# Optimization experiments

Measured on AMD Instinct MI355X. Metric: run time of the kernel, lower is better.

Reference implementation:

```python
import jax, jax.numpy as jnp
import numpy as np

# --- model dims (ModelArgs defaults) ---
DIM = 1024      # model dim
NH = 12         # n_heads
NOPE = 128      # qk_nope_head_dim
ROPE = 64       # qk_rope_head_dim (32 complex pairs)
QKH = NOPE + ROPE  # 192
VH = 128        # v_head_dim
KVR = 512       # kv_lora_rank
B, S = 4, 2048
EPS = 1e-6
SM_SCALE = QKH ** -0.5  # max_seq_len <= original_seq_len -> no mscale


def setup_inputs() -> dict:
    key = jax.random.key(0)
    ks = jax.random.split(key, 6)
    std = lambda fan_in: 0.02 / np.sqrt(fan_in)
    x = jax.random.normal(ks[0], (B, S, DIM), jnp.float32)
    wq = jax.random.normal(ks[1], (NH * QKH, DIM), jnp.float32) * std(DIM)
    wkv_a = jax.random.normal(ks[2], (KVR + ROPE, DIM), jnp.float32) * std(DIM)
    kv_norm_w = jnp.ones((KVR,), jnp.float32)
    wkv_b = jax.random.normal(ks[3], (NH * (NOPE + VH), KVR), jnp.float32) * std(KVR)
    wo = jax.random.normal(ks[4], (DIM, NH * VH), jnp.float32) * std(NH * VH)
    # rotary freqs_cis for positions [0, S): cos/sin of pos * theta^(-2i/ROPE)
    inv_freq = 1.0 / (10000.0 ** (np.arange(0, ROPE, 2, dtype=np.float32) / ROPE))
    ang = np.outer(np.arange(S, dtype=np.float32), inv_freq)  # [S, 32]
    freqs_cis = jnp.stack([jnp.cos(ang), jnp.sin(ang)], axis=-1).astype(jnp.float32)  # [S,32,2]
    # causal mask [S, S]: -inf above diagonal
    i = jnp.arange(S)
    mask = jnp.where(i[None, :] > i[:, None], -jnp.inf, 0.0).astype(jnp.float32)
    return {"x": x, "wq": wq, "wkv_a": wkv_a, "kv_norm_w": kv_norm_w,
            "wkv_b": wkv_b, "wo": wo, "freqs_cis": freqs_cis, "mask": mask,
            "start_pos": 0}


def rmsnorm(x, w, eps=EPS):
    xf = x.astype(jnp.float32)
    return (xf * jax.lax.rsqrt(jnp.mean(xf * xf, axis=-1, keepdims=True) + eps) * w).astype(x.dtype)


def apply_rope(x, freqs_cis):
    # x: [B, S, H, D]; pairs are consecutive last-dim elements (view_as_complex semantics)
    x2 = x.reshape(*x.shape[:-1], -1, 2)
    xr, xi = x2[..., 0], x2[..., 1]
    fr = freqs_cis[..., 0][None, :, None, :]  # [1, S, 1, D/2]
    fi = freqs_cis[..., 1][None, :, None, :]
    yr = xr * fr - xi * fi
    yi = xr * fi + xi * fr
    return jnp.stack([yr, yi], axis=-1).reshape(x.shape).astype(x.dtype)


def reference(x, wq, wkv_a, kv_norm_w, wkv_b, wo, freqs_cis, mask, start_pos):
    bsz, seqlen, _ = x.shape
    # q projection (q_lora_rank == 0 path)
    q = (x @ wq.T).reshape(bsz, seqlen, NH, QKH)
    q_nope, q_pe = q[..., :NOPE], q[..., NOPE:]
    q_pe = apply_rope(q_pe, freqs_cis)
    # low-rank kv projection
    kv_full = x @ wkv_a.T                       # [B,S,KVR+ROPE]
    kv, k_pe = kv_full[..., :KVR], kv_full[..., KVR:]
    k_pe = apply_rope(k_pe[:, :, None, :], freqs_cis)[:, :, 0, :]  # [B,S,ROPE]
    # absorb k-side of wkv_b into q (MLA absorption)
    wkv_b3 = wkv_b.reshape(NH, NOPE + VH, KVR)
    q_nope = jnp.einsum('bshd,hdc->bshc', q_nope, wkv_b3[:, :NOPE])  # [B,S,H,KVR]
    # latent caches (detached in original module)
    kv_c = jax.lax.stop_gradient(rmsnorm(kv, kv_norm_w))  # [B,S,KVR]
    pe_c = jax.lax.stop_gradient(k_pe)                    # [B,S,ROPE]
    scores = (jnp.einsum('bshc,btc->bsht', q_nope, kv_c)
              + jnp.einsum('bshr,btr->bsht', q_pe, pe_c)) * SM_SCALE
    scores = scores + mask[None, :, None, :]
    attn = jax.nn.softmax(scores.astype(jnp.float32), axis=-1).astype(x.dtype)
    o = jnp.einsum('bsht,btc->bshc', attn, kv_c)           # [B,S,H,KVR]
    o = jnp.einsum('bshc,hdc->bshd', o, wkv_b3[:, NOPE:])  # [B,S,H,VH]
    return o.reshape(bsz, seqlen, NH * VH) @ wo.T           # [B,S,DIM]
```

## Files before the change

### kernel.cpp

```cpp
#include <hip/hip_runtime.h>

typedef __bf16 bf16;
typedef __bf16 bf16x8 __attribute__((ext_vector_type(8)));
typedef __bf16 bf16x4 __attribute__((ext_vector_type(4)));
typedef float floatx4 __attribute__((ext_vector_type(4)));

#define T_TOK 8192
#define SEQ 2048
#define KLD 584
#define SM_SCALE 0.07216878364870323f

__device__ __forceinline__ void dma16(const void* g, void* l) {
  __builtin_amdgcn_global_load_lds(
      (const __attribute__((address_space(1))) unsigned int*)g,
      (__attribute__((address_space(3))) unsigned int*)l, 16, 0, 0);
}

__global__ __launch_bounds__(256) void cast_f32_bf16(const float* __restrict__ in,
                                                     bf16* __restrict__ out, long n4) {
  long i = (long)blockIdx.x * 256 + threadIdx.x;
  if (i >= n4) return;
  float4 v = ((const float4*)in)[i];
  bf16x4 o;
  o[0] = (bf16)v.x; o[1] = (bf16)v.y; o[2] = (bf16)v.z; o[3] = (bf16)v.w;
  ((bf16x4*)out)[i] = o;
}

__global__ __launch_bounds__(256) void cast_wkva_pad(const float* __restrict__ in,
                                                     bf16* __restrict__ out) {
  long i = (long)blockIdx.x * 256 + threadIdx.x;
  int r = (int)(i >> 8);
  bf16x4 o;
  if (r < 576) {
    float4 v = ((const float4*)in)[i];
    o[0] = (bf16)v.x; o[1] = (bf16)v.y; o[2] = (bf16)v.z; o[3] = (bf16)v.w;
  } else {
    o[0] = (bf16)0.f; o[1] = (bf16)0.f; o[2] = (bf16)0.f; o[3] = (bf16)0.f;
  }
  ((bf16x4*)out)[i] = o;
}

__global__ __launch_bounds__(256) void split_wkvb(const float* __restrict__ in,
                                                  bf16* __restrict__ wbnT,
                                                  bf16* __restrict__ wbv) {
  int i = blockIdx.x * 256 + threadIdx.x;
  int h = i >> 17, rem = i & 131071, d = rem >> 9, c = rem & 511;
  bf16 v = (bf16)in[i];
  if (d < 128) wbnT[((h * 512 + c) << 7) + d] = v;
  else         wbv[((h * 128 + (d - 128)) << 9) + c] = v;
}

template <int MODE>
__global__ __launch_bounds__(256) void gemm_bt(
    const bf16* __restrict__ A, const bf16* __restrict__ B, void* __restrict__ Cv,
    int N, int K, int lda, int ldb, int ldc,
    long sA, long sB, long sC,
    const float* __restrict__ freqs, bf16* __restrict__ qn, bf16* __restrict__ qabs) {
  __shared__ alignas(16) bf16 As[128 * 32];
  __shared__ alignas(16) bf16 Bs[128 * 32];
  const int z = blockIdx.z;
  A += (long)z * sA;  B += (long)z * sB;
  const int row0 = blockIdx.y * 128, col0 = blockIdx.x * 128;
  const int tid = threadIdx.x;
  const int w = tid >> 6, l = tid & 63, lm = l & 15, quad = l >> 4;
  const int wr = w >> 1, wc = w & 1;
  floatx4 acc[4][4] = {};

  for (int k0 = 0; k0 < K; k0 += 32) {
    __syncthreads();
#pragma unroll
    for (int i = 0; i < 2; i++) {
      int cid = i * 256 + tid;
      int r = cid >> 2, c8 = (cid & 3) * 8;
      *(bf16x8*)(As + r * 32 + c8) = *(const bf16x8*)(A + (long)(row0 + r) * lda + k0 + c8);
      *(bf16x8*)(Bs + r * 32 + c8) = *(const bf16x8*)(B + (long)(col0 + r) * ldb + k0 + c8);
    }
    __syncthreads();
    bf16x8 af[4], bfr[4];
#pragma unroll
    for (int i = 0; i < 4; i++) {
      af[i]  = *(const bf16x8*)(As + (wr * 64 + i * 16 + lm) * 32 + quad * 8);
      bfr[i] = *(const bf16x8*)(Bs + (wc * 64 + i * 16 + lm) * 32 + quad * 8);
    }
#pragma unroll
    for (int i = 0; i < 4; i++)
#pragma unroll
      for (int j = 0; j < 4; j++)
        acc[i][j] = __builtin_amdgcn_mfma_f32_16x16x32_bf16(af[i], bfr[j], acc[i][j], 0, 0, 0);
  }

#pragma unroll
  for (int i = 0; i < 4; i++) {
#pragma unroll
    for (int j = 0; j < 4; j++) {
#pragma unroll
      for (int r = 0; r < 4; r++) {
        float val = acc[i][j][r];
        float partner = __shfl_xor(val, 1, 64);
        int rr = row0 + wr * 64 + i * 16 + quad * 4 + r;
        int cc = col0 + wc * 64 + j * 16 + lm;
        if (cc < N) {
          if (MODE == 0) {
            ((float*)Cv + (long)z * sC)[(long)rr * ldc + cc] = val;
          } else if (MODE == 1) {
            ((bf16*)Cv + (long)z * sC)[(long)rr * ldc + cc] = (bf16)val;
          } else if (MODE == 3) {
            ((bf16*)Cv + (long)z * sC)[(long)cc * ldc + rr] = (bf16)val;
          } else {
            int s = rr & (SEQ - 1);
            int h = cc / 192, wi = cc % 192;
            if (wi < 128) {
              qn[((long)h * T_TOK + rr) * 128 + wi] = (bf16)(val * SM_SCALE);
            } else {
              int pp = (wi - 128) >> 1;
              float cs = freqs[s * 64 + pp * 2], sn = freqs[s * 64 + pp * 2 + 1];
              float res = ((wi & 1) == 0) ? (val * cs - partner * sn)
                                          : (partner * sn + val * cs);
              qabs[((long)h * T_TOK + rr) * 576 + 512 + (wi - 128)] = (bf16)(res * SM_SCALE);
            }
          }
        }
      }
    }
  }
}

__global__ __launch_bounds__(64) void kvnorm_rope(const float* __restrict__ kvf,
                                                  const float* __restrict__ wnorm,
                                                  const float* __restrict__ freqs,
                                                  bf16* __restrict__ Kp) {
  const int t = blockIdx.x, l = threadIdx.x, s = t & (SEQ - 1);
  const float* row = kvf + (long)t * 576;
  float4 a4 = ((const float4*)row)[l * 2];
  float4 b4 = ((const float4*)row)[l * 2 + 1];
  float v[8] = {a4.x, a4.y, a4.z, a4.w, b4.x, b4.y, b4.z, b4.w};
  float ssq = 0.f;
#pragma unroll
  for (int i = 0; i < 8; i++) ssq += v[i] * v[i];
#pragma unroll
  for (int m = 1; m < 64; m <<= 1) ssq += __shfl_xor(ssq, m, 64);
  const float rn = rsqrtf(ssq * (1.f / 512.f) + 1e-6f);
  bf16x8 o;
#pragma unroll
  for (int i = 0; i < 8; i++) o[i] = (bf16)(v[i] * rn * wnorm[l * 8 + i]);
  *(bf16x8*)(Kp + (long)t * KLD + l * 8) = o;
  if (l < 32) {
    float xr = row[512 + 2 * l], xi = row[513 + 2 * l];
    float cs = freqs[s * 64 + 2 * l], sn = freqs[s * 64 + 2 * l + 1];
    Kp[(long)t * KLD + 512 + 2 * l] = (bf16)(xr * cs - xi * sn);
    Kp[(long)t * KLD + 513 + 2 * l] = (bf16)(xr * sn + xi * cs);
  }
}

__global__ __launch_bounds__(256, 3) void mla_attn(const bf16* __restrict__ qabs,
                                                   const bf16* __restrict__ Kp,
                                                   const bf16* __restrict__ VpT,
                                                   bf16* __restrict__ o_all) {
  constexpr int PROW = 40;
  __shared__ alignas(16) bf16 Ks[19456];
  __shared__ alignas(16) bf16 Ps[64 * PROW];
  __shared__ float alpha_s[64];
  __shared__ float l_s[64];

  const int g = blockIdx.y, b = blockIdx.z;
  const int tid = threadIdx.x, w = tid >> 6, l = tid & 63;
  const int lm = l & 15, quad = l >> 4;
  const int h = g * 4 + w;

  const bf16* KpB = Kp + (long)b * SEQ * KLD;

  for (int half = 0; half < 2; half++) {
    const int qt = half ? (int)blockIdx.x : 127 - (int)blockIdx.x;
    const long tq0 = (long)b * SEQ + qt * 16;
    const int nk = (qt >> 1) + 1;
    const int moff = (qt & 1) * 16;

    bf16x8 qf[18];
    {
      const bf16* qb = qabs + ((long)h * T_TOK + tq0 + lm) * 576 + quad * 8;
#pragma unroll
      for (int kk = 0; kk < 18; kk++) qf[kk] = *(const bf16x8*)(qb + kk * 32);
    }
    floatx4 oacc[4][2] = {};
    float mstate = -__builtin_inff(), lstate = 0.f;

    if (half == 0) {
      const char* gk = (const char*)KpB;
      for (int j = w; j < 37; j += 4)
        dma16(gk + j * 1024 + l * 16, (char*)Ks + j * 1024);
    }
    __syncthreads();

    for (int kt = 0; kt < nk; kt++) {
      floatx4 sacc[2] = {};
#pragma unroll
      for (int kk = 0; kk < 18; kk++) {
        bf16x8 kf0 = *(const bf16x8*)(Ks + lm * KLD + kk * 32 + quad * 8);
        bf16x8 kf1 = *(const bf16x8*)(Ks + (16 + lm) * KLD + kk * 32 + quad * 8);
        sacc[0] = __builtin_amdgcn_mfma_f32_16x16x32_bf16(kf0, qf[kk], sacc[0], 0, 0, 0);
        sacc[1] = __builtin_amdgcn_mfma_f32_16x16x32_bf16(kf1, qf[kk], sacc[1], 0, 0, 0);
      }
      if (kt == nk - 1) {
#pragma unroll
        for (int i = 0; i < 2; i++)
#pragma unroll
          for (int r = 0; r < 4; r++)
            if (i * 16 + quad * 4 + r > moff + lm) sacc[i][r] = -__builtin_inff();
      }
      float cmax = -__builtin_inff();
#pragma unroll
      for (int i = 0; i < 2; i++)
#pragma unroll
        for (int r = 0; r < 4; r++) cmax = fmaxf(cmax, sacc[i][r]);
      cmax = fmaxf(cmax, __shfl_xor(cmax, 16, 64));
      cmax = fmaxf(cmax, __shfl_xor(cmax, 32, 64));
      const float mnew = fmaxf(mstate, cmax);
      const float alpha = __expf(mstate - mnew);
      float psum = 0.f;
#pragma unroll
      for (int i = 0; i < 2; i++) {
        bf16x4 pw;
#pragma unroll
        for (int r = 0; r < 4; r++) {
          float pv = __expf(sacc[i][r] - mnew);
          psum += pv;
          pw[r] = (bf16)pv;
        }
        *(bf16x4*)(Ps + (w * 16 + lm) * PROW + i * 16 + quad * 4) = pw;
      }
      psum += __shfl_xor(psum, 16, 64);
      psum += __shfl_xor(psum, 32, 64);
      lstate = lstate * alpha + psum;
      mstate = mnew;
      if (l < 16) alpha_s[w * 16 + l] = alpha;
      __syncthreads();

      if (kt + 1 < nk) {
        const char* gk = (const char*)(KpB + (long)(kt + 1) * 32 * KLD);
        for (int j = w; j < 37; j += 4)
          dma16(gk + j * 1024 + l * 16, (char*)Ks + j * 1024);
      } else if (half == 0) {
        const char* gk = (const char*)KpB;
        for (int j = w; j < 37; j += 4)
          dma16(gk + j * 1024 + l * 16, (char*)Ks + j * 1024);
      }

#pragma unroll
      for (int mi = 0; mi < 4; mi++) {
#pragma unroll
        for (int r = 0; r < 4; r++) {
          const float a = alpha_s[mi * 16 + quad * 4 + r];
          oacc[mi][0][r] *= a;
          oacc[mi][1][r] *= a;
        }
      }
      const long tv = (long)b * SEQ + kt * 32 + quad * 8;
#pragma unroll
      for (int mi = 0; mi < 4; mi++) {
        const bf16* vrow = VpT + ((long)((g * 4 + mi) * 128 + w * 32 + lm)) * T_TOK + tv;
        bf16x8 vb0 = *(const bf16x8*)(vrow);
        bf16x8 vb1 = *(const bf16x8*)(vrow + (long)16 * T_TOK);
        bf16x8 pa = *(const bf16x8*)(Ps + (mi * 16 + lm) * PROW + quad * 8);
        oacc[mi][0] = __builtin_amdgcn_mfma_f32_16x16x32_bf16(pa, vb0, oacc[mi][0], 0, 0, 0);
        oacc[mi][1] = __builtin_amdgcn_mfma_f32_16x16x32_bf16(pa, vb1, oacc[mi][1], 0, 0, 0);
      }
      __syncthreads();
    }

    if (l < 16) l_s[w * 16 + l] = lstate;
    __syncthreads();
#pragma unroll
    for (int mi = 0; mi < 4; mi++) {
#pragma unroll
      for (int r = 0; r < 4; r++) {
        const int qrow = quad * 4 + r;
        const float inv = 1.f / l_s[mi * 16 + qrow];
#pragma unroll
        for (int nj = 0; nj < 2; nj++)
          o_all[(tq0 + qrow) * 1536 + (g * 4 + mi) * 128 + w * 32 + nj * 16 + lm] =
              (bf16)(oacc[mi][nj][r] * inv);
      }
    }
  }
}

extern "C" void kernel_launch(void* const* d_in, const int* in_sizes, int n_in,
                              void* d_out, int out_size, void* d_ws, size_t ws_size,
                              hipStream_t stream) {
  (void)in_sizes; (void)n_in; (void)out_size; (void)ws_size;
  const float* x     = (const float*)d_in[0];
  const float* wq    = (const float*)d_in[1];
  const float* wkva  = (const float*)d_in[2];
  const float* kvnw  = (const float*)d_in[3];
  const float* wkvb  = (const float*)d_in[4];
  const float* wo    = (const float*)d_in[5];
  const float* freqs = (const float*)d_in[6];
  float* out = (float*)d_out;

  char* p = (char*)d_ws;
  auto alloc = [&](size_t bytes) {
    char* r = p;
    p += (bytes + 255) & ~(size_t)255;
    return r;
  };
  bf16*  xb    = (bf16*) alloc((size_t)T_TOK * 1024 * 2);
  bf16*  wqb   = (bf16*) alloc((size_t)2304 * 1024 * 2);
  bf16*  wkvab = (bf16*) alloc((size_t)640 * 1024 * 2);
  bf16*  wbnT  = (bf16*) alloc((size_t)12 * 512 * 128 * 2);
  bf16*  wbv   = (bf16*) alloc((size_t)12 * 128 * 512 * 2);
  bf16*  wob   = (bf16*) alloc((size_t)1024 * 1536 * 2);
  float* kvf   = (float*)alloc((size_t)T_TOK * 576 * 4);
  bf16*  Kp    = (bf16*) alloc((size_t)T_TOK * KLD * 2 + 4096);
  bf16*  VpT   = (bf16*) alloc((size_t)12 * 128 * T_TOK * 2);
  bf16*  qn    = (bf16*) alloc((size_t)12 * T_TOK * 128 * 2);
  bf16*  qabs  = (bf16*) alloc((size_t)12 * T_TOK * 576 * 2);
  bf16*  o_all = (bf16*) alloc((size_t)T_TOK * 1536 * 2);

  cast_f32_bf16<<<8192, 256, 0, stream>>>(x, xb, (long)T_TOK * 1024 / 4);
  cast_f32_bf16<<<2304, 256, 0, stream>>>(wq, wqb, (long)2304 * 1024 / 4);
  cast_wkva_pad<<<640, 256, 0, stream>>>(wkva, wkvab);
  split_wkvb<<<6144, 256, 0, stream>>>(wkvb, wbnT, wbv);
  cast_f32_bf16<<<1536, 256, 0, stream>>>(wo, wob, (long)1024 * 1536 / 4);

  gemm_bt<0><<<dim3(5, 64, 1), 256, 0, stream>>>(xb, wkvab, (void*)kvf, 576, 1024,
      1024, 1024, 576, 0, 0, 0, nullptr, nullptr, nullptr);
  gemm_bt<2><<<dim3(18, 64, 1), 256, 0, stream>>>(xb, wqb, nullptr, 2304, 1024,
      1024, 1024, 0, 0, 0, 0, freqs, qn, qabs);
  kvnorm_rope<<<T_TOK, 64, 0, stream>>>(kvf, kvnw, freqs, Kp);
  gemm_bt<3><<<dim3(1, 64, 12), 256, 0, stream>>>(Kp, wbv, (void*)VpT, 128, 512,
      KLD, 512, T_TOK, 0, (long)128 * 512, (long)128 * T_TOK,
      nullptr, nullptr, nullptr);
  gemm_bt<1><<<dim3(4, 64, 12), 256, 0, stream>>>(qn, wbnT, (void*)qabs, 512, 128,
      128, 128, 576, (long)T_TOK * 128, (long)512 * 128, (long)T_TOK * 576,
      nullptr, nullptr, nullptr);
  mla_attn<<<dim3(64, 3, 4), 256, 0, stream>>>(qabs, Kp, VpT, o_all);
  gemm_bt<0><<<dim3(8, 64, 1), 256, 0, stream>>>(o_all, wob, (void*)out, 1024, 1536,
      1536, 1536, 1024, 0, 0, 0, nullptr, nullptr, nullptr);
}
```

Before: 712.9 us.

## Prefetch V fragments early, swizzle block order across XCDs, unroll K DMA

```diff
diff --git a/kernel.cpp b/kernel.cpp
--- a/kernel.cpp
+++ b/kernel.cpp
@@ -157,12 +157,17 @@
                                                    const bf16* __restrict__ VpT,
                                                    bf16* __restrict__ o_all) {
   constexpr int PROW = 40;
-  __shared__ alignas(16) bf16 Ks[19456];
+  __shared__ alignas(16) bf16 Ks[20480];
   __shared__ alignas(16) bf16 Ps[64 * PROW];
   __shared__ float alpha_s[64];
   __shared__ float l_s[64];
 
-  const int g = blockIdx.y, b = blockIdx.z;
+  const int p = blockIdx.x + 64 * (blockIdx.y + 3 * blockIdx.z);
+  const int lid = (p & 7) * 96 + (p >> 3);
+  const int b = lid / 192;
+  const int rgx = lid % 192;
+  const int g = rgx >> 6, qx = rgx & 63;
+
   const int tid = threadIdx.x, w = tid >> 6, l = tid & 63;
   const int lm = l & 15, quad = l >> 4;
   const int h = g * 4 + w;
@@ -170,7 +175,7 @@
   const bf16* KpB = Kp + (long)b * SEQ * KLD;
 
   for (int half = 0; half < 2; half++) {
-    const int qt = half ? (int)blockIdx.x : 127 - (int)blockIdx.x;
+    const int qt = half ? qx : 127 - qx;
     const long tq0 = (long)b * SEQ + qt * 16;
     const int nk = (qt >> 1) + 1;
     const int moff = (qt & 1) * 16;
@@ -186,12 +191,22 @@
 
     if (half == 0) {
       const char* gk = (const char*)KpB;
-      for (int j = w; j < 37; j += 4)
-        dma16(gk + j * 1024 + l * 16, (char*)Ks + j * 1024);
+#pragma unroll
+      for (int jj = 0; jj < 10; jj++)
+        dma16(gk + (w + jj * 4) * 1024 + l * 16, (char*)Ks + (w + jj * 4) * 1024);
     }
     __syncthreads();
 
     for (int kt = 0; kt < nk; kt++) {
+      bf16x8 vb[4][2];
+      const long tv = (long)b * SEQ + kt * 32 + quad * 8;
+#pragma unroll
+      for (int mi = 0; mi < 4; mi++) {
+        const bf16* vrow = VpT + ((long)((g * 4 + mi) * 128 + w * 32 + lm)) * T_TOK + tv;
+        vb[mi][0] = *(const bf16x8*)(vrow);
+        vb[mi][1] = *(const bf16x8*)(vrow + (long)16 * T_TOK);
+      }
+
       floatx4 sacc[2] = {};
 #pragma unroll
       for (int kk = 0; kk < 18; kk++) {
@@ -235,14 +250,12 @@
       if (l < 16) alpha_s[w * 16 + l] = alpha;
       __syncthreads();
 
-      if (kt + 1 < nk) {
-        const char* gk = (const char*)(KpB + (long)(kt + 1) * 32 * KLD);
-        for (int j = w; j < 37; j += 4)
-          dma16(gk + j * 1024 + l * 16, (char*)Ks + j * 1024);
-      } else if (half == 0) {
-        const char* gk = (const char*)KpB;
-        for (int j = w; j < 37; j += 4)
-          dma16(gk + j * 1024 + l * 16, (char*)Ks + j * 1024);
+      {
+        const int ktn = (kt + 1 < nk) ? kt + 1 : (half == 0 ? 0 : kt);
+        const char* gk = (const char*)(KpB + (long)ktn * 32 * KLD);
+#pragma unroll
+        for (int jj = 0; jj < 10; jj++)
+          dma16(gk + (w + jj * 4) * 1024 + l * 16, (char*)Ks + (w + jj * 4) * 1024);
       }
 
 #pragma unroll
@@ -254,15 +267,11 @@
           oacc[mi][1][r] *= a;
         }
       }
-      const long tv = (long)b * SEQ + kt * 32 + quad * 8;
 #pragma unroll
       for (int mi = 0; mi < 4; mi++) {
-        const bf16* vrow = VpT + ((long)((g * 4 + mi) * 128 + w * 32 + lm)) * T_TOK + tv;
-        bf16x8 vb0 = *(const bf16x8*)(vrow);
-        bf16x8 vb1 = *(const bf16x8*)(vrow + (long)16 * T_TOK);
         bf16x8 pa = *(const bf16x8*)(Ps + (mi * 16 + lm) * PROW + quad * 8);
-        oacc[mi][0] = __builtin_amdgcn_mfma_f32_16x16x32_bf16(pa, vb0, oacc[mi][0], 0, 0, 0);
-        oacc[mi][1] = __builtin_amdgcn_mfma_f32_16x16x32_bf16(pa, vb1, oacc[mi][1], 0, 0, 0);
+        oacc[mi][0] = __builtin_amdgcn_mfma_f32_16x16x32_bf16(pa, vb[mi][0], oacc[mi][0], 0, 0, 0);
+        oacc[mi][1] = __builtin_amdgcn_mfma_f32_16x16x32_bf16(pa, vb[mi][1], oacc[mi][1], 0, 0, 0);
       }
       __syncthreads();
     }
```

Measured after the change: 753.5 us. 5.7% more time.
